# Optimization experiments

Hardware: AMD Instinct MI355X
Metric: run time of the kernel (lower is better)

Reference implementation:

```python
import jax, jax.numpy as jnp
import numpy as np

# ---- MMAL-Net canonical configuration (baked constants of the module) ----
STRIDE = 32          # backbone stride: feature cell -> input pixels
FM = 14              # feature-map side (448 / 32)
RATIOS = [[4, 4], [3, 5], [5, 3],
          [6, 6], [5, 7], [7, 5],
          [8, 8], [6, 10], [10, 6], [7, 9], [9, 7]]
GROUP_SLICES = [(0, 3), (3, 6), (6, 11)]   # 3 scale groups of ratios
N_LIST = [3, 2, 1]                          # proposals kept per group
IOU_THRESHS = [0.25, 0.25, 0.25]


def _make_coords():
    # pixel-space [x0, y0, x1, y1] per sliding window, row-major (i outer, j inner)
    # matching the row-major flatten of the pooled feature maps.
    c = []
    for rh, rw in RATIOS:
        for i in range(FM - rh + 1):
            for j in range(FM - rw + 1):
                c.append([j * STRIDE, i * STRIDE,
                          (j + rw) * STRIDE - 1, (i + rh) * STRIDE - 1])
    return jnp.asarray(np.array(c, np.float32))

COORDS = _make_coords()                                   # [837, 4]
WIN_NUMS = [(FM - rh + 1) * (FM - rw + 1) for rh, rw in RATIOS]
GROUP_WINS = [sum(WIN_NUMS[a:b]) for a, b in GROUP_SLICES]  # [361, 241, 235]
GROUP_OFFSETS = [0, GROUP_WINS[0], GROUP_WINS[0] + GROUP_WINS[1]]
TOTAL_WINS = sum(GROUP_WINS)                              # 837


def _window_scores(x):
    """sum_c avgpool(x, r) == avgpool(sum_c x, r) -- fuse the channel reduction
    first so we avoid materializing [B, C, h', w'] per ratio."""
    y = jnp.sum(x, axis=1)  # [B, H, W]
    parts = []
    for rh, rw in RATIOS:
        s = jax.lax.reduce_window(y, jnp.float32(0), jax.lax.add,
                                  (1, rh, rw), (1, 1, 1), 'VALID') / (rh * rw)
        parts.append(s.reshape(y.shape[0], -1))
    return jnp.concatenate(parts, axis=1)  # [B, TOTAL_WINS]


def _nms_group(scores, coords, n_sel, iou_thresh):
    """Greedy NMS on one scale group: fixed n_sel iterations of
    (argmax over surviving windows, suppress IoU > thresh). If candidates run
    out, the last selected index is repeated (matches the torch fallback)."""
    W = scores.shape[0]
    area = (coords[:, 2] - coords[:, 0] + 1.) * (coords[:, 3] - coords[:, 1] + 1.)

    def step(carry, _):
        valid, last = carry
        any_v = jnp.any(valid)
        idx = jnp.argmax(jnp.where(valid, scores, -jnp.inf))
        idx = jnp.where(any_v, idx, last)
        sel = coords[idx]
        lt = jnp.maximum(coords[:, :2], sel[:2])
        rb = jnp.minimum(coords[:, 2:], sel[2:])
        wh = rb - lt + 1.
        inter = jnp.where((wh[:, 0] < 0) | (wh[:, 1] < 0), 0., wh[:, 0] * wh[:, 1])
        iou = inter / (area + area[idx] - inter)
        new_valid = (valid & (iou <= iou_thresh)).at[idx].set(False)
        new_valid = jnp.where(any_v, new_valid, valid)
        return (new_valid, idx), idx

    (_, _), sel = jax.lax.scan(step, (jnp.ones(W, bool), jnp.int32(0)),
                               None, length=n_sel)
    return sel  # [n_sel] int32 local indices


def setup_inputs() -> dict:
    key = jax.random.key(0)
    x = jax.random.normal(key, (64, 2048, FM, FM), dtype=jnp.float32)
    return {"x": x, "proposalN": 6}


def reference(x, proposalN):
    all_scores = _window_scores(x)  # [B, 837]
    idx_parts = []
    for g in range(len(N_LIST)):
        off, W = GROUP_OFFSETS[g], GROUP_WINS[g]
        sc = all_scores[:, off:off + W]
        co = COORDS[off:off + W]
        sel = jax.vmap(lambda s: _nms_group(s, co, N_LIST[g], IOU_THRESHS[g]))(sc)
        idx_parts.append(sel + off)
    proposal_indices = jnp.concatenate(idx_parts, axis=1)  # [B, proposalN]
    proposal_scores = jnp.take_along_axis(all_scores, proposal_indices, axis=1)
    return proposal_indices, proposal_scores, all_scores
```

## Files before the change

### kernel.cpp

```cpp
#include <hip/hip_runtime.h>
#include <math.h>

#define B 64
#define C 2048
#define FMH 14
#define HW 196
#define HW4 49
#define CHUNKS 32
#define CPC (C / CHUNKS)
#define NWIN 837

__device__ __constant__ int d_RH[11]   = {4, 3, 5, 6, 5, 7, 8, 6, 10, 7, 9};
__device__ __constant__ int d_RW[11]   = {4, 5, 3, 6, 7, 5, 8, 10, 6, 9, 7};
__device__ __constant__ int d_WOFF[12] = {0, 121, 241, 361, 442, 522, 602, 651, 696, 741, 789, 837};

__global__ __launch_bounds__(256) void sum_channels_kernel(const float4* __restrict__ x,
                                                           float4* __restrict__ partial) {
    const int chunk = blockIdx.x;
    const int b     = blockIdx.y;
    const int lane  = threadIdx.x & 63;
    const int wave  = threadIdx.x >> 6;

    float4 acc = make_float4(0.f, 0.f, 0.f, 0.f);
    if (lane < HW4) {
        const float4* base = x + (size_t)(b * C + chunk * CPC) * HW4 + lane;
        #pragma unroll 4
        for (int k = 0; k < CPC / 4; ++k) {
            float4 v = base[(size_t)(wave + 4 * k) * HW4];
            acc.x += v.x; acc.y += v.y; acc.z += v.z; acc.w += v.w;
        }
    }

    __shared__ float4 sh[256];
    sh[threadIdx.x] = acc;
    __syncthreads();

    if (threadIdx.x < 64 && lane < HW4) {
        float4 a0 = sh[lane], a1 = sh[64 + lane], a2 = sh[128 + lane], a3 = sh[192 + lane];
        float4 s;
        s.x = (a0.x + a1.x) + (a2.x + a3.x);
        s.y = (a0.y + a1.y) + (a2.y + a3.y);
        s.z = (a0.z + a1.z) + (a2.z + a3.z);
        s.w = (a0.w + a1.w) + (a2.w + a3.w);
        partial[(size_t)(b * CHUNKS + chunk) * HW4 + lane] = s;
    }
}

__device__ inline void decode_box(int w, float& x0, float& y0, float& x1, float& y1, float& area) {
    int r = 0;
    while (w >= d_WOFF[r + 1]) ++r;
    int local = w - d_WOFF[r];
    int rh = d_RH[r], rw = d_RW[r];
    int wc = FMH - rw + 1;
    int i = local / wc, j = local - i * wc;
    x0 = (float)(j * 32);
    y0 = (float)(i * 32);
    x1 = (float)((j + rw) * 32 - 1);
    y1 = (float)((i + rh) * 32 - 1);
    area = (float)(rw * 32) * (float)(rh * 32);
}

__global__ __launch_bounds__(256) void scores_nms_kernel(const float* __restrict__ partial,
                                                         float* __restrict__ out) {
    const int b   = blockIdx.x;
    const int tid = threadIdx.x;

    __shared__ float S[15][16];
    __shared__ float sc[NWIN];
    __shared__ unsigned char valid[384];
    __shared__ float redv[256];
    __shared__ int   redi[256];
    __shared__ int   s_sel, s_any;
    __shared__ float s_box[4];
    __shared__ float s_area;

    if (tid < HW) {
        const float* p = partial + (size_t)b * CHUNKS * HW + tid;
        float acc = 0.f;
        #pragma unroll
        for (int ch = 0; ch < CHUNKS; ++ch) acc += p[(size_t)ch * HW];
        S[tid / FMH + 1][tid % FMH + 1] = acc;
    }
    if (tid < 16) S[0][tid] = 0.f;
    if (tid < 15) S[tid][0] = 0.f;
    __syncthreads();

    if (tid < 14) {
        float r = 0.f;
        for (int j = 1; j <= 14; ++j) { r += S[tid + 1][j]; S[tid + 1][j] = r; }
    }
    __syncthreads();
    if (tid < 14) {
        int j = tid + 1;
        float r = 0.f;
        for (int i = 1; i <= 14; ++i) { r += S[i][j]; S[i][j] = r; }
    }
    __syncthreads();

    for (int w = tid; w < NWIN; w += 256) {
        int r = 0;
        while (w >= d_WOFF[r + 1]) ++r;
        int local = w - d_WOFF[r];
        int rh = d_RH[r], rw = d_RW[r];
        int wc = FMH - rw + 1;
        int i = local / wc, j = local - i * wc;
        float s = (S[i + rh][j + rw] - S[i][j + rw] - S[i + rh][j] + S[i][j]) / (float)(rh * rw);
        sc[w] = s;
        out[768 + (size_t)b * NWIN + w] = s;
    }
    __syncthreads();

    const int GOFF[3] = {0, 361, 602};
    const int GW_[3]  = {361, 241, 235};
    const int NSEL[3] = {3, 2, 1};
    int slot = 0;
    for (int g = 0; g < 3; ++g) {
        const int off = GOFF[g], W = GW_[g];
        for (int wl = tid; wl < W; wl += 256) valid[wl] = 1;
        __syncthreads();
        int last = 0;
        for (int it = 0; it < NSEL[g]; ++it) {
            float bv = -INFINITY; int bi = 0x7fffffff;
            for (int wl = tid; wl < W; wl += 256) {
                if (valid[wl]) {
                    float v = sc[off + wl];
                    if (v > bv || (v == bv && wl < bi)) { bv = v; bi = wl; }
                }
            }
            redv[tid] = bv; redi[tid] = bi;
            __syncthreads();
            for (int s = 128; s > 0; s >>= 1) {
                if (tid < s) {
                    if (redv[tid + s] > redv[tid] ||
                        (redv[tid + s] == redv[tid] && redi[tid + s] < redi[tid])) {
                        redv[tid] = redv[tid + s]; redi[tid] = redi[tid + s];
                    }
                }
                __syncthreads();
            }
            if (tid == 0) {
                int any = (redv[0] != -INFINITY) ? 1 : 0;
                int sel = any ? redi[0] : last;
                s_any = any; s_sel = sel;
                float x0, y0, x1, y1, area;
                decode_box(off + sel, x0, y0, x1, y1, area);
                s_box[0] = x0; s_box[1] = y0; s_box[2] = x1; s_box[3] = y1; s_area = area;
                out[(size_t)b * 6 + slot]       = (float)(off + sel);
                out[384 + (size_t)b * 6 + slot] = sc[off + sel];
            }
            __syncthreads();
            const int sel = s_sel;
            last = sel;
            if (s_any) {
                const float sx0 = s_box[0], sy0 = s_box[1], sx1 = s_box[2], sy1 = s_box[3];
                const float sa = s_area;
                for (int wl = tid; wl < W; wl += 256) {
                    if (!valid[wl]) continue;
                    float x0, y0, x1, y1, area;
                    decode_box(off + wl, x0, y0, x1, y1, area);
                    float ltx = fmaxf(x0, sx0), lty = fmaxf(y0, sy0);
                    float rbx = fminf(x1, sx1), rby = fminf(y1, sy1);
                    float wx = rbx - ltx + 1.f, wy = rby - lty + 1.f;
                    float inter = (wx < 0.f || wy < 0.f) ? 0.f : wx * wy;
                    float iou = inter / (area + sa - inter);
                    if (iou > 0.25f) valid[wl] = 0;
                }
                if (tid == 0) valid[sel] = 0;
            }
            __syncthreads();
            ++slot;
        }
    }
}

extern "C" void kernel_launch(void* const* d_in, const int* in_sizes, int n_in,
                              void* d_out, int out_size, void* d_ws, size_t ws_size,
                              hipStream_t stream) {
    const float* x = (const float*)d_in[0];
    float* out = (float*)d_out;
    float* partial = (float*)d_ws;

    sum_channels_kernel<<<dim3(CHUNKS, B), 256, 0, stream>>>((const float4*)x, (float4*)partial);
    scores_nms_kernel<<<B, 256, 0, stream>>>(partial, out);
}
```

Measured before the change: 169.3 us.

## Run NMS kernel as a single wavefront with register masks and shuffle argmax

```diff
diff --git a/kernel.cpp b/kernel.cpp
--- a/kernel.cpp
+++ b/kernel.cpp
@@ -9,6 +9,7 @@
 #define CHUNKS 32
 #define CPC (C / CHUNKS)
 #define NWIN 837
+#define KMAX 6
 
 __device__ __constant__ int d_RH[11]   = {4, 3, 5, 6, 5, 7, 8, 6, 10, 7, 9};
 __device__ __constant__ int d_RW[11]   = {4, 5, 3, 6, 7, 5, 8, 10, 6, 9, 7};
@@ -60,44 +61,48 @@
     area = (float)(rw * 32) * (float)(rh * 32);
 }
 
-__global__ __launch_bounds__(256) void scores_nms_kernel(const float* __restrict__ partial,
-                                                         float* __restrict__ out) {
-    const int b   = blockIdx.x;
-    const int tid = threadIdx.x;
+__global__ __launch_bounds__(64) void scores_nms_kernel(const float* __restrict__ partial,
+                                                        float* __restrict__ out) {
+    const int b    = blockIdx.x;
+    const int lane = threadIdx.x;
 
     __shared__ float S[15][16];
     __shared__ float sc[NWIN];
-    __shared__ unsigned char valid[384];
-    __shared__ float redv[256];
-    __shared__ int   redi[256];
-    __shared__ int   s_sel, s_any;
-    __shared__ float s_box[4];
-    __shared__ float s_area;
 
-    if (tid < HW) {
-        const float* p = partial + (size_t)b * CHUNKS * HW + tid;
-        float acc = 0.f;
+    {
+        float a0 = 0.f, a1 = 0.f, a2 = 0.f, a3 = 0.f;
+        const float* p = partial + (size_t)b * CHUNKS * HW;
         #pragma unroll
-        for (int ch = 0; ch < CHUNKS; ++ch) acc += p[(size_t)ch * HW];
-        S[tid / FMH + 1][tid % FMH + 1] = acc;
+        for (int ch = 0; ch < CHUNKS; ++ch) {
+            const float* q = p + ch * HW;
+            a0 += q[lane];
+            a1 += q[64 + lane];
+            a2 += q[128 + lane];
+            if (lane < 4) a3 += q[192 + lane];
+        }
+        int h0 = lane, h1 = 64 + lane, h2 = 128 + lane;
+        S[h0 / FMH + 1][h0 % FMH + 1] = a0;
+        S[h1 / FMH + 1][h1 % FMH + 1] = a1;
+        S[h2 / FMH + 1][h2 % FMH + 1] = a2;
+        if (lane < 4) { int h3 = 192 + lane; S[h3 / FMH + 1][h3 % FMH + 1] = a3; }
+        if (lane < 16) S[0][lane] = 0.f;
+        if (lane < 15) S[lane][0] = 0.f;
     }
-    if (tid < 16) S[0][tid] = 0.f;
-    if (tid < 15) S[tid][0] = 0.f;
     __syncthreads();
 
-    if (tid < 14) {
+    if (lane < 14) {
         float r = 0.f;
-        for (int j = 1; j <= 14; ++j) { r += S[tid + 1][j]; S[tid + 1][j] = r; }
+        for (int j = 1; j <= 14; ++j) { r += S[lane + 1][j]; S[lane + 1][j] = r; }
     }
     __syncthreads();
-    if (tid < 14) {
-        int j = tid + 1;
+    if (lane < 14) {
+        int j = lane + 1;
         float r = 0.f;
         for (int i = 1; i <= 14; ++i) { r += S[i][j]; S[i][j] = r; }
     }
     __syncthreads();
 
-    for (int w = tid; w < NWIN; w += 256) {
+    for (int w = lane; w < NWIN; w += 64) {
         int r = 0;
         while (w >= d_WOFF[r + 1]) ++r;
         int local = w - d_WOFF[r];
@@ -116,58 +121,61 @@
     int slot = 0;
     for (int g = 0; g < 3; ++g) {
         const int off = GOFF[g], W = GW_[g];
-        for (int wl = tid; wl < W; wl += 256) valid[wl] = 1;
-        __syncthreads();
+
+        float sv[KMAX], bx0[KMAX], by0[KMAX], bx1[KMAX], by1[KMAX], bar[KMAX];
+        unsigned vmask = 0;
+        #pragma unroll
+        for (int k = 0; k < KMAX; ++k) {
+            int wl = lane + 64 * k;
+            if (wl < W) {
+                sv[k] = sc[off + wl];
+                decode_box(off + wl, bx0[k], by0[k], bx1[k], by1[k], bar[k]);
+                vmask |= (1u << k);
+            } else {
+                sv[k] = -INFINITY;
+            }
+        }
+
         int last = 0;
         for (int it = 0; it < NSEL[g]; ++it) {
             float bv = -INFINITY; int bi = 0x7fffffff;
-            for (int wl = tid; wl < W; wl += 256) {
-                if (valid[wl]) {
-                    float v = sc[off + wl];
+            #pragma unroll
+            for (int k = 0; k < KMAX; ++k) {
+                if (vmask & (1u << k)) {
+                    float v = sv[k];
+                    int wl = lane + 64 * k;
                     if (v > bv || (v == bv && wl < bi)) { bv = v; bi = wl; }
                 }
             }
-            redv[tid] = bv; redi[tid] = bi;
-            __syncthreads();
-            for (int s = 128; s > 0; s >>= 1) {
-                if (tid < s) {
-                    if (redv[tid + s] > redv[tid] ||
-                        (redv[tid + s] == redv[tid] && redi[tid + s] < redi[tid])) {
-                        redv[tid] = redv[tid + s]; redi[tid] = redi[tid + s];
-                    }
-                }
-                __syncthreads();
+            #pragma unroll
+            for (int d = 1; d < 64; d <<= 1) {
+                float ov = __shfl_xor(bv, d, 64);
+                int   oi = __shfl_xor(bi, d, 64);
+                if (ov > bv || (ov == bv && oi < bi)) { bv = ov; bi = oi; }
             }
-            if (tid == 0) {
-                int any = (redv[0] != -INFINITY) ? 1 : 0;
-                int sel = any ? redi[0] : last;
-                s_any = any; s_sel = sel;
-                float x0, y0, x1, y1, area;
-                decode_box(off + sel, x0, y0, x1, y1, area);
-                s_box[0] = x0; s_box[1] = y0; s_box[2] = x1; s_box[3] = y1; s_area = area;
+            const bool any = (bv != -INFINITY);
+            const int sel = any ? bi : last;
+            last = sel;
+            if (lane == 0) {
                 out[(size_t)b * 6 + slot]       = (float)(off + sel);
                 out[384 + (size_t)b * 6 + slot] = sc[off + sel];
             }
-            __syncthreads();
-            const int sel = s_sel;
-            last = sel;
-            if (s_any) {
-                const float sx0 = s_box[0], sy0 = s_box[1], sx1 = s_box[2], sy1 = s_box[3];
-                const float sa = s_area;
-                for (int wl = tid; wl < W; wl += 256) {
-                    if (!valid[wl]) continue;
-                    float x0, y0, x1, y1, area;
-                    decode_box(off + wl, x0, y0, x1, y1, area);
-                    float ltx = fmaxf(x0, sx0), lty = fmaxf(y0, sy0);
-                    float rbx = fminf(x1, sx1), rby = fminf(y1, sy1);
-                    float wx = rbx - ltx + 1.f, wy = rby - lty + 1.f;
-                    float inter = (wx < 0.f || wy < 0.f) ? 0.f : wx * wy;
-                    float iou = inter / (area + sa - inter);
-                    if (iou > 0.25f) valid[wl] = 0;
+            if (any) {
+                float sx0, sy0, sx1, sy1, sa;
+                decode_box(off + sel, sx0, sy0, sx1, sy1, sa);
+                #pragma unroll
+                for (int k = 0; k < KMAX; ++k) {
+                    if (vmask & (1u << k)) {
+                        float ltx = fmaxf(bx0[k], sx0), lty = fmaxf(by0[k], sy0);
+                        float rbx = fminf(bx1[k], sx1), rby = fminf(by1[k], sy1);
+                        float wx = rbx - ltx + 1.f, wy = rby - lty + 1.f;
+                        float inter = (wx < 0.f || wy < 0.f) ? 0.f : wx * wy;
+                        float iou = inter / (bar[k] + sa - inter);
+                        if (iou > 0.25f) vmask &= ~(1u << k);
+                    }
                 }
-                if (tid == 0) valid[sel] = 0;
+                if ((sel & 63) == lane) vmask &= ~(1u << (sel >> 6));
             }
-            __syncthreads();
             ++slot;
         }
     }
@@ -181,5 +189,5 @@
     float* partial = (float*)d_ws;
 
     sum_channels_kernel<<<dim3(CHUNKS, B), 256, 0, stream>>>((const float4*)x, (float4*)partial);
-    scores_nms_kernel<<<B, 256, 0, stream>>>(partial, out);
+    scores_nms_kernel<<<B, 64, 0, stream>>>(partial, out);
 }
```

New measurement: 179.3 us. 1.06x slower.
